# Optimization experiments

Measured on AMD Instinct MI355X. Metric: run time of the kernel, lower is better.

## Reference

```python
import jax, jax.numpy as jnp
import numpy as np

N = 8192          # nodes in batch
D_IN = 512        # in_channels
G = 512           # global_dim
D_OUT = 512       # out_channels
H = 8             # heads
C = 2048          # num_centroids
NUM_NODES = 100000


def setup_inputs() -> dict:
    key = jax.random.key(0)
    ks = jax.random.split(key, 10)
    s = lambda fan_in: 1.0 / np.sqrt(fan_in)
    return {
        "x": jax.random.normal(ks[0], (N, D_IN), jnp.float32),
        "W_proj": jax.random.normal(ks[1], (D_IN, G), jnp.float32) * s(D_IN),
        "b_proj": jnp.zeros((G,), jnp.float32),
        "W_q": jax.random.normal(ks[2], (G, D_OUT), jnp.float32) * s(G),
        "b_q": jnp.zeros((D_OUT,), jnp.float32),
        "W_k": jax.random.normal(ks[3], (G, D_OUT), jnp.float32) * s(G),
        "b_k": jnp.zeros((D_OUT,), jnp.float32),
        "W_v": jax.random.normal(ks[4], (G, D_OUT), jnp.float32) * s(G),
        "b_v": jnp.zeros((D_OUT,), jnp.float32),
        "k_buf": jax.random.normal(ks[5], (C, G), jnp.float32),
        "v_buf": jax.random.normal(ks[6], (C, G), jnp.float32),
        "ln_gamma": jnp.ones((D_OUT,), jnp.float32),
        "ln_beta": jnp.zeros((D_OUT,), jnp.float32),
        "c_idx": jax.random.randint(ks[7], (NUM_NODES,), 0, C, jnp.int64 if jax.config.jax_enable_x64 else jnp.int32),
        "node_indices": jax.random.randint(ks[8], (N,), 0, NUM_NODES, jnp.int64 if jax.config.jax_enable_x64 else jnp.int32),
    }


def _layer_norm(y, gamma, beta, eps=1e-5):
    mu = jnp.mean(y, axis=-1, keepdims=True)
    var = jnp.var(y, axis=-1, keepdims=True)
    return (y - mu) * jax.lax.rsqrt(var + eps) * gamma + beta


def reference(x, W_proj, b_proj, W_q, b_q, W_k, b_k, W_v, b_v,
              k_buf, v_buf, ln_gamma, ln_beta, c_idx, node_indices):
    h, d = H, D_OUT
    dh = d // h
    scale = 1.0 / np.sqrt(d)  # source scales by 1/sqrt(out_channels)

    q_x = x @ W_proj + b_proj                      # [N, G]
    k_x = jax.lax.stop_gradient(k_buf)             # detach().clone()
    v_x = jax.lax.stop_gradient(v_buf)

    # n (h d) -> h n d
    q = (q_x @ W_q + b_q).reshape(-1, h, dh).transpose(1, 0, 2)   # [h, N, dh]
    k = (k_x @ W_k + b_k).reshape(-1, h, dh).transpose(1, 0, 2)   # [h, C, dh]
    v = (v_x @ W_v + b_v).reshape(-1, h, dh).transpose(1, 0, 2)   # [h, C, dh]

    dots = jnp.einsum('hnd,hcd->hnc', q, k) * scale               # [h, N, C]

    # log-count centroid bias (unique/bincount over the full c_idx buffer)
    counts = jnp.bincount(c_idx, length=C)                        # [C] int
    dots = dots + jnp.log(counts.astype(dots.dtype))              # log(0)=-inf masks empty centroids

    attn = jax.nn.softmax(dots, axis=-1)                          # [h, N, C]
    out = jnp.einsum('hnc,hcd->hnd', attn, v)                     # [h, N, dh]
    out = out.transpose(1, 0, 2).reshape(-1, d)                   # [N, d]

    return _layer_norm(out, ln_gamma, ln_beta)
```

## Files before the change

### kernel.cpp

```cpp
#include <hip/hip_runtime.h>
#include <math.h>

typedef __bf16 bf16x8 __attribute__((ext_vector_type(8)));
typedef __bf16 bf16x2 __attribute__((ext_vector_type(2)));
typedef float f32x4 __attribute__((ext_vector_type(4)));
typedef float f32x16 __attribute__((ext_vector_type(16)));
typedef unsigned u32x2v __attribute__((ext_vector_type(2)));
typedef unsigned short u16;

#define NQ 8192
#define DMODEL 512
#define NHEAD 8
#define DH 64
#define NC 2048
#define NIDX 100000

__device__ __forceinline__ u16 f2bf(float f) {
    unsigned u = __float_as_uint(f);
    u += 0x7fffu + ((u >> 16) & 1u);
    return (u16)(u >> 16);
}
__device__ __forceinline__ float bf2f(u16 h) {
    return __uint_as_float(((unsigned)h) << 16);
}
__device__ __forceinline__ unsigned pk2(float a, float b) {
    bf16x2 t; t[0] = (__bf16)a; t[1] = (__bf16)b;
    return __builtin_bit_cast(unsigned, t);
}
__device__ __forceinline__ void plswap(unsigned& a, unsigned& b) {
    u32x2v r = __builtin_amdgcn_permlane32_swap(a, b, false, false);
    a = r[0]; b = r[1];
}
__device__ __forceinline__ int soff(int q, int col) {
    return q * 256 + ((((col >> 2) ^ (q & 7)) << 2) | (col & 3));
}

template <int A_MODE, int B_MODE, int OUT_T>
__device__ __forceinline__ void gemm_bt_body(
    const void* __restrict__ A_, const void* __restrict__ Bt_,
    const float* __restrict__ bias, u16* __restrict__ Cmat,
    int M, int N, int K, int bx, int by)
{
    constexpr int LDP = 40;
    __shared__ __align__(16) u16 As[128 * LDP];
    __shared__ __align__(16) u16 Bs[128 * LDP];
    int tid = threadIdx.x;
    int lane = tid & 63, wid = tid >> 6;
    int wrow = (wid >> 1) * 64, wcol = (wid & 1) * 64;
    int m0 = by * 128, n0 = bx * 128;
    int lr = lane & 15, lg = lane >> 4;
    f32x4 acc[4][4] = {};

    for (int k0 = 0; k0 < K; k0 += 32) {
#pragma unroll
        for (int c = 0; c < 2; c++) {
            int ch = tid + c * 256;
            int row = ch >> 2, colc = (ch & 3) * 8;
            uint4 av;
            if (A_MODE == 1) {
                const float* Af = (const float*)A_;
                float4 a0 = *(const float4*)(Af + (size_t)(m0 + row) * K + k0 + colc);
                float4 a1 = *(const float4*)(Af + (size_t)(m0 + row) * K + k0 + colc + 4);
                av.x = pk2(a0.x, a0.y); av.y = pk2(a0.z, a0.w);
                av.z = pk2(a1.x, a1.y); av.w = pk2(a1.z, a1.w);
            } else if (A_MODE == 2) {
                const float* Af = (const float*)A_;
                float e[8];
#pragma unroll
                for (int i = 0; i < 8; i++)
                    e[i] = Af[(size_t)(k0 + colc + i) * M + m0 + row];
                av.x = pk2(e[0], e[1]); av.y = pk2(e[2], e[3]);
                av.z = pk2(e[4], e[5]); av.w = pk2(e[6], e[7]);
            } else {
                av = *(const uint4*)((const u16*)A_ + (size_t)(m0 + row) * K + k0 + colc);
            }
            *(uint4*)(&As[row * LDP + colc]) = av;
            uint4 bv;
            if (B_MODE == 1) {
                const float* Bf = (const float*)Bt_;
                float4 b0 = *(const float4*)(Bf + (size_t)(n0 + row) * K + k0 + colc);
                float4 b1 = *(const float4*)(Bf + (size_t)(n0 + row) * K + k0 + colc + 4);
                bv.x = pk2(b0.x, b0.y); bv.y = pk2(b0.z, b0.w);
                bv.z = pk2(b1.x, b1.y); bv.w = pk2(b1.z, b1.w);
            } else {
                bv = *(const uint4*)((const u16*)Bt_ + (size_t)(n0 + row) * K + k0 + colc);
            }
            *(uint4*)(&Bs[row * LDP + colc]) = bv;
        }
        __syncthreads();
        bf16x8 af[4], bfr[4];
#pragma unroll
        for (int m = 0; m < 4; m++)
            af[m] = *(const bf16x8*)(&As[(wrow + m * 16 + lr) * LDP + lg * 8]);
#pragma unroll
        for (int n = 0; n < 4; n++)
            bfr[n] = *(const bf16x8*)(&Bs[(wcol + n * 16 + lr) * LDP + lg * 8]);
#pragma unroll
        for (int m = 0; m < 4; m++)
#pragma unroll
            for (int n = 0; n < 4; n++)
                acc[m][n] = __builtin_amdgcn_mfma_f32_16x16x32_bf16(af[m], bfr[n], acc[m][n], 0, 0, 0);
        __syncthreads();
    }
#pragma unroll
    for (int n = 0; n < 4; n++) {
        int col = n0 + wcol + n * 16 + lr;
        float bv = bias ? bias[col] : 0.0f;
#pragma unroll
        for (int m = 0; m < 4; m++) {
            int rbase = m0 + wrow + m * 16 + lg * 4;
            if (OUT_T == 1) {
                int hh = col >> 6, T = (col >> 5) & 1, ql = col & 31;
                int t = rbase >> 5, cc = rbase & 31;
                int u = ((cc >> 4) * 2 + ((cc >> 3) & 1)) * 2 + T;
                size_t off = (size_t)hh * 131072 + (size_t)t * 2048 + u * 256 + ql * 8 + (cc & 7);
                ushort4 o4;
                o4.x = f2bf(acc[m][n][0] + bv);
                o4.y = f2bf(acc[m][n][1] + bv);
                o4.z = f2bf(acc[m][n][2] + bv);
                o4.w = f2bf(acc[m][n][3] + bv);
                *(ushort4*)(Cmat + off) = o4;
            } else if (OUT_T == 2) {
                int hh = col >> 6, m2 = (col >> 4) & 3, h2 = (col >> 3) & 1, jj = col & 7;
                size_t ub = (size_t)hh * 131072 + (size_t)(m2 * 2 + h2) * 256 + jj;
#pragma unroll
                for (int r = 0; r < 4; r++) {
                    int c = rbase + r;
                    Cmat[ub + (size_t)(c >> 5) * 2048 + (c & 31) * 8] = f2bf(acc[m][n][r] + bv);
                }
            } else {
#pragma unroll
                for (int r = 0; r < 4; r++)
                    Cmat[(size_t)(rbase + r) * N + col] = f2bf(acc[m][n][r] + bv);
            }
        }
    }
}

__global__ __launch_bounds__(256) void k_prep2(
    const float* __restrict__ Wq, const float* __restrict__ Wk, const float* __restrict__ Wv,
    const float* __restrict__ Wp, const float* __restrict__ bp, const float* __restrict__ bq_,
    u16* __restrict__ Wk_t, u16* __restrict__ Wv_t,
    u16* __restrict__ WcombT, float* __restrict__ bcomb)
{
    __shared__ float tile[32][33];
    int bid = blockIdx.x, tid = threadIdx.x;
    if (bid < 16) {
        gemm_bt_body<2, 1, 0>(Wq, Wp, nullptr, WcombT, DMODEL, DMODEL, DMODEL,
                              bid & 3, bid >> 2);
    } else if (bid < 18) {
        int j = (bid - 16) * 256 + tid;
        float s = bq_[j];
        for (int k = 0; k < DMODEL; k++) s += bp[k] * Wq[(size_t)k * DMODEL + j];
        bcomb[j] = s;
    } else {
        const float* W; u16* Wt; int tb;
        if (bid < 274) { W = Wk; Wt = Wk_t; tb = bid - 18; }
        else           { W = Wv; Wt = Wv_t; tb = bid - 274; }
        int c0 = (tb & 15) * 32, r0 = (tb >> 4) * 32;
        int tx = tid & 31, ty = tid >> 5;
#pragma unroll
        for (int i = 0; i < 4; i++)
            tile[ty + i * 8][tx] = W[(size_t)(r0 + ty + i * 8) * DMODEL + c0 + tx];
        __syncthreads();
#pragma unroll
        for (int i = 0; i < 4; i++)
            Wt[(size_t)(c0 + ty + i * 8) * DMODEL + r0 + tx] = f2bf(tile[tx][ty + i * 8]);
    }
}

__global__ __launch_bounds__(256) void k_gemm_all(
    const float* __restrict__ kb, const u16* __restrict__ Wkt, const float* __restrict__ bk,
    u16* __restrict__ Kp,
    const float* __restrict__ vb, const u16* __restrict__ Wvt, const float* __restrict__ bv,
    u16* __restrict__ Vp,
    const float* __restrict__ x, const u16* __restrict__ WcombT,
    const float* __restrict__ bcomb, u16* __restrict__ Qm,
    const int* __restrict__ cidx, int* __restrict__ counts)
{
    int b = blockIdx.x;
    if (b < 64)
        gemm_bt_body<1, 0, 2>(kb, Wkt, bk, Kp, NC, DMODEL, DMODEL, b & 3, b >> 2);
    else if (b < 128)
        gemm_bt_body<1, 0, 1>(vb, Wvt, bv, Vp, NC, DMODEL, DMODEL, (b - 64) & 3, (b - 64) >> 2);
    else if (b < 384)
        gemm_bt_body<1, 0, 0>(x, WcombT, bcomb, Qm, NQ, DMODEL, DMODEL, (b - 128) & 3, (b - 128) >> 2);
    else {
        for (int i = (b - 384) * 256 + threadIdx.x; i < NIDX; i += 128 * 256)
            atomicAdd(&counts[cidx[i]], 1);
    }
}

__global__ __launch_bounds__(512, 2) void k_attn8(
    const u16* __restrict__ Q, const u16* __restrict__ Kp, const u16* __restrict__ Vp,
    const int* __restrict__ counts, const float* __restrict__ ln_g,
    const float* __restrict__ ln_b, float* __restrict__ Out, float scale2)
{
    __shared__ float sbias[NC];
    __shared__ unsigned sO[32 * 256];

    int tid = threadIdx.x;
    int lane = tid & 63, wid = tid >> 6;
    int h = wid;
    int ql = lane & 31, hi = lane >> 5;
    int q0 = blockIdx.x * 32;
    int hbase = h * DH;

#pragma unroll
    for (int i = 0; i < 4; i++)
        sbias[tid + i * 512] = log2f((float)counts[tid + i * 512]) - 16.0f;

    bf16x8 qf[4];
#pragma unroll
    for (int m = 0; m < 4; m++)
        qf[m] = *(const bf16x8*)(Q + (size_t)(q0 + ql) * DMODEL + hbase + m * 16 + hi * 8);

    const u16* klane = Kp + (size_t)h * 131072 + hi * 256 + ql * 8;
    const u16* vlane = Vp + (size_t)h * 131072 + hi * 512 + ql * 8;

    bf16x8 kf0[4], kf1[4], vf0[4], vf1[4];
#pragma unroll
    for (int m = 0; m < 4; m++)
        kf0[m] = *(const bf16x8*)(klane + m * 512);
#pragma unroll
    for (int T = 0; T < 2; T++)
#pragma unroll
        for (int ss = 0; ss < 2; ss++)
            vf0[T * 2 + ss] = *(const bf16x8*)(vlane + ss * 1024 + T * 256);

    f32x16 o0 = {}, o1 = {};
    float l_part = 0.f;

    __syncthreads();

    auto body = [&](int t, bf16x8 (&kfc)[4], bf16x8 (&vfc)[4],
                    bf16x8 (&kfn)[4], bf16x8 (&vfn)[4]) {
        f32x4 bq[4];
#pragma unroll
        for (int j = 0; j < 4; j++)
            bq[j] = *(const f32x4*)(sbias + t * 32 + 8 * j + 4 * hi);

        f32x16 acc = {};
        __builtin_amdgcn_s_setprio(1);
#pragma unroll
        for (int m = 0; m < 4; m++)
            acc = __builtin_amdgcn_mfma_f32_32x32x16_bf16(kfc[m], qf[m], acc, 0, 0, 0);
        __builtin_amdgcn_s_setprio(0);

        const u16* kp = klane + (size_t)(t + 1) * 2048;
#pragma unroll
        for (int m = 0; m < 4; m++)
            kfn[m] = *(const bf16x8*)(kp + m * 512);

        unsigned u[8];
        float rs0 = 0.f, rs1 = 0.f;
#pragma unroll
        for (int j = 0; j < 8; j++) {
            float p0 = exp2f(acc[2 * j] * scale2 + bq[(2 * j) >> 2][(2 * j) & 3]);
            float p1 = exp2f(acc[2 * j + 1] * scale2 + bq[(2 * j + 1) >> 2][(2 * j + 1) & 3]);
            rs0 += p0; rs1 += p1;
            u[j] = pk2(p0, p1);
        }
        l_part += rs0 + rs1;

        plswap(u[0], u[2]); plswap(u[1], u[3]);
        plswap(u[4], u[6]); plswap(u[5], u[7]);
        bf16x8 pb0 = __builtin_bit_cast(bf16x8, *(uint4*)&u[0]);
        bf16x8 pb1 = __builtin_bit_cast(bf16x8, *(uint4*)&u[4]);

        __builtin_amdgcn_s_setprio(1);
        o0 = __builtin_amdgcn_mfma_f32_32x32x16_bf16(vfc[0], pb0, o0, 0, 0, 0);
        o0 = __builtin_amdgcn_mfma_f32_32x32x16_bf16(vfc[1], pb1, o0, 0, 0, 0);
        o1 = __builtin_amdgcn_mfma_f32_32x32x16_bf16(vfc[2], pb0, o1, 0, 0, 0);
        o1 = __builtin_amdgcn_mfma_f32_32x32x16_bf16(vfc[3], pb1, o1, 0, 0, 0);
        __builtin_amdgcn_s_setprio(0);

        const u16* vp = vlane + (size_t)(t + 1) * 2048;
#pragma unroll
        for (int T = 0; T < 2; T++)
#pragma unroll
            for (int ss = 0; ss < 2; ss++)
                vfn[T * 2 + ss] = *(const bf16x8*)(vp + ss * 1024 + T * 256);
    };

    for (int t = 0; t < NC / 32; t += 2) {
        body(t,     kf0, vf0, kf1, vf1);
        body(t + 1, kf1, vf1, kf0, vf0);
    }

    float l_tot = l_part + __shfl_xor(l_part, 32);
    float inv = 1.0f / l_tot;

#pragma unroll
    for (int T = 0; T < 2; T++)
#pragma unroll
        for (int j = 0; j < 8; j++) {
            int dw = T * 16 + (j & 1) + 4 * (j >> 1) + 2 * hi;
            float a = (T == 0) ? o0[2 * j] : o1[2 * j];
            float b = (T == 0) ? o0[2 * j + 1] : o1[2 * j + 1];
            sO[soff(ql, h * 32 + dw)] = pk2(a * inv, b * inv);
        }
    __syncthreads();

    float4 g0 = *(const float4*)(ln_g + lane * 8);
    float4 g1 = *(const float4*)(ln_g + lane * 8 + 4);
    float4 b0 = *(const float4*)(ln_b + lane * 8);
    float4 b1 = *(const float4*)(ln_b + lane * 8 + 4);
#pragma unroll
    for (int rr = 0; rr < 4; rr++) {
        int r = wid * 4 + rr;
        uint4 pw = *(const uint4*)(&sO[r * 256 + ((lane ^ (r & 7)) << 2)]);
        float v[8];
        v[0] = bf2f((u16)(pw.x & 0xffff)); v[1] = bf2f((u16)(pw.x >> 16));
        v[2] = bf2f((u16)(pw.y & 0xffff)); v[3] = bf2f((u16)(pw.y >> 16));
        v[4] = bf2f((u16)(pw.z & 0xffff)); v[5] = bf2f((u16)(pw.z >> 16));
        v[6] = bf2f((u16)(pw.w & 0xffff)); v[7] = bf2f((u16)(pw.w >> 16));
        float sum = 0.f, sq = 0.f;
#pragma unroll
        for (int j = 0; j < 8; j++) { sum += v[j]; sq += v[j] * v[j]; }
#pragma unroll
        for (int msk = 1; msk <= 32; msk <<= 1) { sum += __shfl_xor(sum, msk); sq += __shfl_xor(sq, msk); }
        float mu = sum * (1.f / DMODEL);
        float var = sq * (1.f / DMODEL) - mu * mu;
        float rstd = rsqrtf(var + 1e-5f);
        float o[8];
        o[0] = (v[0] - mu) * rstd * g0.x + b0.x; o[1] = (v[1] - mu) * rstd * g0.y + b0.y;
        o[2] = (v[2] - mu) * rstd * g0.z + b0.z; o[3] = (v[3] - mu) * rstd * g0.w + b0.w;
        o[4] = (v[4] - mu) * rstd * g1.x + b1.x; o[5] = (v[5] - mu) * rstd * g1.y + b1.y;
        o[6] = (v[6] - mu) * rstd * g1.z + b1.z; o[7] = (v[7] - mu) * rstd * g1.w + b1.w;
        float* op = Out + (size_t)(q0 + r) * DMODEL + lane * 8;
        *(float4*)op = *(float4*)&o[0];
        *(float4*)(op + 4) = *(float4*)&o[4];
    }
}

extern "C" void kernel_launch(void* const* d_in, const int* in_sizes, int n_in,
                              void* d_out, int out_size, void* d_ws, size_t ws_size,
                              hipStream_t stream)
{
    const float* x      = (const float*)d_in[0];
    const float* W_proj = (const float*)d_in[1];
    const float* b_proj = (const float*)d_in[2];
    const float* W_q    = (const float*)d_in[3];
    const float* b_q    = (const float*)d_in[4];
    const float* W_k    = (const float*)d_in[5];
    const float* b_k    = (const float*)d_in[6];
    const float* W_v    = (const float*)d_in[7];
    const float* b_v    = (const float*)d_in[8];
    const float* k_buf  = (const float*)d_in[9];
    const float* v_buf  = (const float*)d_in[10];
    const float* ln_g   = (const float*)d_in[11];
    const float* ln_b   = (const float*)d_in[12];
    const int*   c_idx  = (const int*)d_in[13];
    float* out = (float*)d_out;

    char* ws = (char*)d_ws;
    size_t off = 0;
    auto alloc = [&](size_t bytes) -> void* {
        void* p = ws + off;
        off += (bytes + 255) & ~(size_t)255;
        return p;
    };
    u16* Wk_t   = (u16*)alloc((size_t)DMODEL * DMODEL * 2);
    u16* Wv_t   = (u16*)alloc((size_t)DMODEL * DMODEL * 2);
    u16* WcombT = (u16*)alloc((size_t)DMODEL * DMODEL * 2);
    u16* Qm     = (u16*)alloc((size_t)NQ * DMODEL * 2);
    u16* Kpm    = (u16*)alloc((size_t)NC * DMODEL * 2);
    u16* Vpm    = (u16*)alloc((size_t)DMODEL * NC * 2);
    int*   counts = (int*)alloc(NC * 4);
    float* bcomb  = (float*)alloc(DMODEL * 4);
    (void)alloc(2200000);

    hipMemsetAsync(counts, 0, NC * 4, stream);

    k_prep2<<<dim3(530), dim3(256), 0, stream>>>(
        W_q, W_k, W_v, W_proj, b_proj, b_q,
        Wk_t, Wv_t, WcombT, bcomb);

    k_gemm_all<<<dim3(512), dim3(256), 0, stream>>>(
        k_buf, Wk_t, b_k, Kpm,
        v_buf, Wv_t, b_v, Vpm,
        x, WcombT, bcomb, Qm,
        c_idx, counts);

    k_attn8<<<dim3(NQ / 32), dim3(512), 0, stream>>>(Qm, Kpm, Vpm, counts, ln_g, ln_b, out, 0.06375872f);
    (void)in_sizes; (void)n_in; (void)out_size; (void)ws_size;
}
```

Baseline: 124.9 us.

## Split centroid dimension across two wave groups per head in attention kernel

Doubles the attention block to 1024 threads so each head gets two waves, each covering half of the 2048 centroids. The partial outputs and row sums are merged through shared memory before normalization and layer norm. This raises the wave count and parallelism per query tile, at the cost of extra shared-memory traffic, more barriers and a bf16-rounded partial sum.

```diff
diff --git a/kernel.cpp b/kernel.cpp
--- a/kernel.cpp
+++ b/kernel.cpp
@@ -191,32 +191,33 @@
     }
 }
 
-__global__ __launch_bounds__(512, 2) void k_attn8(
+__global__ __launch_bounds__(1024, 4) void k_attn9(
     const u16* __restrict__ Q, const u16* __restrict__ Kp, const u16* __restrict__ Vp,
     const int* __restrict__ counts, const float* __restrict__ ln_g,
     const float* __restrict__ ln_b, float* __restrict__ Out, float scale2)
 {
     __shared__ float sbias[NC];
     __shared__ unsigned sO[32 * 256];
+    __shared__ float sl[256];
 
     int tid = threadIdx.x;
     int lane = tid & 63, wid = tid >> 6;
-    int h = wid;
+    int h = wid & 7, hf = wid >> 3;
     int ql = lane & 31, hi = lane >> 5;
     int q0 = blockIdx.x * 32;
     int hbase = h * DH;
 
-#pragma unroll
-    for (int i = 0; i < 4; i++)
-        sbias[tid + i * 512] = log2f((float)counts[tid + i * 512]) - 16.0f;
+    sbias[tid] = log2f((float)counts[tid]) - 16.0f;
+    sbias[tid + 1024] = log2f((float)counts[tid + 1024]) - 16.0f;
 
     bf16x8 qf[4];
 #pragma unroll
     for (int m = 0; m < 4; m++)
         qf[m] = *(const bf16x8*)(Q + (size_t)(q0 + ql) * DMODEL + hbase + m * 16 + hi * 8);
 
-    const u16* klane = Kp + (size_t)h * 131072 + hi * 256 + ql * 8;
-    const u16* vlane = Vp + (size_t)h * 131072 + hi * 512 + ql * 8;
+    const u16* klane = Kp + (size_t)h * 131072 + (size_t)hf * 65536 + hi * 256 + ql * 8;
+    const u16* vlane = Vp + (size_t)h * 131072 + (size_t)hf * 65536 + hi * 512 + ql * 8;
+    int bbase = hf * 1024;
 
     bf16x8 kf0[4], kf1[4], vf0[4], vf1[4];
 #pragma unroll
@@ -238,7 +239,7 @@
         f32x4 bq[4];
 #pragma unroll
         for (int j = 0; j < 4; j++)
-            bq[j] = *(const f32x4*)(sbias + t * 32 + 8 * j + 4 * hi);
+            bq[j] = *(const f32x4*)(sbias + bbase + t * 32 + 8 * j + 4 * hi);
 
         f32x16 acc = {};
         __builtin_amdgcn_s_setprio(1);
@@ -283,23 +284,53 @@
                 vfn[T * 2 + ss] = *(const bf16x8*)(vp + ss * 1024 + T * 256);
     };
 
-    for (int t = 0; t < NC / 32; t += 2) {
+    for (int t = 0; t < NC / 64; t += 2) {
         body(t,     kf0, vf0, kf1, vf1);
         body(t + 1, kf1, vf1, kf0, vf0);
     }
 
     float l_tot = l_part + __shfl_xor(l_part, 32);
-    float inv = 1.0f / l_tot;
-
-#pragma unroll
-    for (int T = 0; T < 2; T++)
-#pragma unroll
-        for (int j = 0; j < 8; j++) {
-            int dw = T * 16 + (j & 1) + 4 * (j >> 1) + 2 * hi;
-            float a = (T == 0) ? o0[2 * j] : o1[2 * j];
-            float b = (T == 0) ? o0[2 * j + 1] : o1[2 * j + 1];
-            sO[soff(ql, h * 32 + dw)] = pk2(a * inv, b * inv);
-        }
+
+    if (hf == 1) {
+#pragma unroll
+        for (int T = 0; T < 2; T++)
+#pragma unroll
+            for (int j = 0; j < 8; j++) {
+                int dw = T * 16 + (j & 1) + 4 * (j >> 1) + 2 * hi;
+                float a = (T == 0) ? o0[2 * j] : o1[2 * j];
+                float b = (T == 0) ? o0[2 * j + 1] : o1[2 * j + 1];
+                sO[(h * 32 + ql) * 32 + dw] = pk2(a, b);
+            }
+        if (hi == 0) sl[h * 32 + ql] = l_tot;
+    }
+    __syncthreads();
+
+    float mrg[32];
+    if (hf == 0) {
+        float inv = 1.0f / (l_tot + sl[h * 32 + ql]);
+#pragma unroll
+        for (int T = 0; T < 2; T++)
+#pragma unroll
+            for (int j = 0; j < 8; j++) {
+                int dw = T * 16 + (j & 1) + 4 * (j >> 1) + 2 * hi;
+                unsigned pv = sO[(h * 32 + ql) * 32 + dw];
+                float a = (T == 0) ? o0[2 * j] : o1[2 * j];
+                float b = (T == 0) ? o0[2 * j + 1] : o1[2 * j + 1];
+                mrg[T * 16 + 2 * j]     = (a + bf2f((u16)(pv & 0xffff))) * inv;
+                mrg[T * 16 + 2 * j + 1] = (b + bf2f((u16)(pv >> 16))) * inv;
+            }
+    }
+    __syncthreads();
+
+    if (hf == 0) {
+#pragma unroll
+        for (int T = 0; T < 2; T++)
+#pragma unroll
+            for (int j = 0; j < 8; j++) {
+                int dw = T * 16 + (j & 1) + 4 * (j >> 1) + 2 * hi;
+                sO[soff(ql, h * 32 + dw)] = pk2(mrg[T * 16 + 2 * j], mrg[T * 16 + 2 * j + 1]);
+            }
+    }
     __syncthreads();
 
     float4 g0 = *(const float4*)(ln_g + lane * 8);
@@ -307,8 +338,8 @@
     float4 b0 = *(const float4*)(ln_b + lane * 8);
     float4 b1 = *(const float4*)(ln_b + lane * 8 + 4);
 #pragma unroll
-    for (int rr = 0; rr < 4; rr++) {
-        int r = wid * 4 + rr;
+    for (int rr = 0; rr < 2; rr++) {
+        int r = wid * 2 + rr;
         uint4 pw = *(const uint4*)(&sO[r * 256 + ((lane ^ (r & 7)) << 2)]);
         float v[8];
         v[0] = bf2f((u16)(pw.x & 0xffff)); v[1] = bf2f((u16)(pw.x >> 16));
@@ -383,6 +414,6 @@
         x, WcombT, bcomb, Qm,
         c_idx, counts);
 
-    k_attn8<<<dim3(NQ / 32), dim3(512), 0, stream>>>(Qm, Kpm, Vpm, counts, ln_g, ln_b, out, 0.06375872f);
+    k_attn9<<<dim3(NQ / 32), dim3(1024), 0, stream>>>(Qm, Kpm, Vpm, counts, ln_g, ln_b, out, 0.06375872f);
     (void)in_sizes; (void)n_in; (void)out_size; (void)ws_size;
 }
```

After: 146.6 us. +17.3%, slower.

## Split attention over centroid halves and merge with separate layernorm kernel

Applied to the files above, without the earlier changes.

Splits the centroid dimension of the attention kernel into two halves via a second grid dimension, doubling the block count. Each half writes unnormalized-by-global partial outputs in bf16 plus row sums, and a new kernel merges the two halves weighted by their sums before applying layernorm. Launch bounds raise the target occupancy to 4 blocks per CU. The aim is better CU utilization with 256 blocks on a many-CU GPU, at the cost of extra global traffic, an extra launch and a second bf16 rounding of the partials. The merge relies on the fixed max bias (no running max), so combining by sums is valid.

```diff
diff --git a/kernel.cpp b/kernel.cpp
--- a/kernel.cpp
+++ b/kernel.cpp
@@ -191,12 +191,12 @@
     }
 }
 
-__global__ __launch_bounds__(512, 2) void k_attn8(
+__global__ __launch_bounds__(512, 4) void k_attn10(
     const u16* __restrict__ Q, const u16* __restrict__ Kp, const u16* __restrict__ Vp,
-    const int* __restrict__ counts, const float* __restrict__ ln_g,
-    const float* __restrict__ ln_b, float* __restrict__ Out, float scale2)
-{
-    __shared__ float sbias[NC];
+    const int* __restrict__ counts, u16* __restrict__ Pp, float* __restrict__ lbuf,
+    float scale2)
+{
+    __shared__ float sbias[NC / 2];
     __shared__ unsigned sO[32 * 256];
 
     int tid = threadIdx.x;
@@ -204,19 +204,19 @@
     int h = wid;
     int ql = lane & 31, hi = lane >> 5;
     int q0 = blockIdx.x * 32;
+    int half = blockIdx.y;
     int hbase = h * DH;
 
-#pragma unroll
-    for (int i = 0; i < 4; i++)
-        sbias[tid + i * 512] = log2f((float)counts[tid + i * 512]) - 16.0f;
+    sbias[tid] = log2f((float)counts[half * 1024 + tid]) - 16.0f;
+    sbias[tid + 512] = log2f((float)counts[half * 1024 + tid + 512]) - 16.0f;
 
     bf16x8 qf[4];
 #pragma unroll
     for (int m = 0; m < 4; m++)
         qf[m] = *(const bf16x8*)(Q + (size_t)(q0 + ql) * DMODEL + hbase + m * 16 + hi * 8);
 
-    const u16* klane = Kp + (size_t)h * 131072 + hi * 256 + ql * 8;
-    const u16* vlane = Vp + (size_t)h * 131072 + hi * 512 + ql * 8;
+    const u16* klane = Kp + (size_t)h * 131072 + (size_t)half * 65536 + hi * 256 + ql * 8;
+    const u16* vlane = Vp + (size_t)h * 131072 + (size_t)half * 65536 + hi * 512 + ql * 8;
 
     bf16x8 kf0[4], kf1[4], vf0[4], vf1[4];
 #pragma unroll
@@ -283,13 +283,16 @@
                 vfn[T * 2 + ss] = *(const bf16x8*)(vp + ss * 1024 + T * 256);
     };
 
-    for (int t = 0; t < NC / 32; t += 2) {
+    for (int t = 0; t < NC / 64; t += 2) {
         body(t,     kf0, vf0, kf1, vf1);
         body(t + 1, kf1, vf1, kf0, vf0);
     }
 
     float l_tot = l_part + __shfl_xor(l_part, 32);
     float inv = 1.0f / l_tot;
+
+    if (hi == 0)
+        lbuf[((size_t)half * NQ + q0 + ql) * NHEAD + h] = l_tot;
 
 #pragma unroll
     for (int T = 0; T < 2; T++)
@@ -302,36 +305,61 @@
         }
     __syncthreads();
 
+#pragma unroll
+    for (int rr = 0; rr < 4; rr++) {
+        int r = wid * 4 + rr;
+        uint4 pw = *(const uint4*)(&sO[r * 256 + ((lane ^ (r & 7)) << 2)]);
+        *(uint4*)(Pp + ((size_t)half * NQ + q0 + r) * DMODEL + lane * 8) = pw;
+    }
+}
+
+__global__ __launch_bounds__(256) void k_mln2(
+    const u16* __restrict__ Pp, const float* __restrict__ lbuf,
+    const float* __restrict__ ln_g, const float* __restrict__ ln_b,
+    float* __restrict__ Out)
+{
+    int lane = threadIdx.x & 63, wid = threadIdx.x >> 6;
+    int q = blockIdx.x * 4 + wid;
+    int hd = lane >> 3;
+
+    float la = lbuf[(size_t)q * NHEAD + hd];
+    float lb = lbuf[((size_t)NQ + q) * NHEAD + hd];
+    float winv = 1.0f / (la + lb);
+    float wa = la * winv, wb = lb * winv;
+
+    uint4 pa = *(const uint4*)(Pp + (size_t)q * DMODEL + lane * 8);
+    uint4 pb = *(const uint4*)(Pp + ((size_t)NQ + q) * DMODEL + lane * 8);
+    float v[8];
+    v[0] = bf2f((u16)(pa.x & 0xffff)) * wa + bf2f((u16)(pb.x & 0xffff)) * wb;
+    v[1] = bf2f((u16)(pa.x >> 16))    * wa + bf2f((u16)(pb.x >> 16))    * wb;
+    v[2] = bf2f((u16)(pa.y & 0xffff)) * wa + bf2f((u16)(pb.y & 0xffff)) * wb;
+    v[3] = bf2f((u16)(pa.y >> 16))    * wa + bf2f((u16)(pb.y >> 16))    * wb;
+    v[4] = bf2f((u16)(pa.z & 0xffff)) * wa + bf2f((u16)(pb.z & 0xffff)) * wb;
+    v[5] = bf2f((u16)(pa.z >> 16))    * wa + bf2f((u16)(pb.z >> 16))    * wb;
+    v[6] = bf2f((u16)(pa.w & 0xffff)) * wa + bf2f((u16)(pb.w & 0xffff)) * wb;
+    v[7] = bf2f((u16)(pa.w >> 16))    * wa + bf2f((u16)(pb.w >> 16))    * wb;
+
+    float sum = 0.f, sq = 0.f;
+#pragma unroll
+    for (int j = 0; j < 8; j++) { sum += v[j]; sq += v[j] * v[j]; }
+#pragma unroll
+    for (int msk = 1; msk <= 32; msk <<= 1) { sum += __shfl_xor(sum, msk); sq += __shfl_xor(sq, msk); }
+    float mu = sum * (1.f / DMODEL);
+    float var = sq * (1.f / DMODEL) - mu * mu;
+    float rstd = rsqrtf(var + 1e-5f);
+
     float4 g0 = *(const float4*)(ln_g + lane * 8);
     float4 g1 = *(const float4*)(ln_g + lane * 8 + 4);
     float4 b0 = *(const float4*)(ln_b + lane * 8);
     float4 b1 = *(const float4*)(ln_b + lane * 8 + 4);
-#pragma unroll
-    for (int rr = 0; rr < 4; rr++) {
-        int r = wid * 4 + rr;
-        uint4 pw = *(const uint4*)(&sO[r * 256 + ((lane ^ (r & 7)) << 2)]);
-        float v[8];
-        v[0] = bf2f((u16)(pw.x & 0xffff)); v[1] = bf2f((u16)(pw.x >> 16));
-        v[2] = bf2f((u16)(pw.y & 0xffff)); v[3] = bf2f((u16)(pw.y >> 16));
-        v[4] = bf2f((u16)(pw.z & 0xffff)); v[5] = bf2f((u16)(pw.z >> 16));
-        v[6] = bf2f((u16)(pw.w & 0xffff)); v[7] = bf2f((u16)(pw.w >> 16));
-        float sum = 0.f, sq = 0.f;
-#pragma unroll
-        for (int j = 0; j < 8; j++) { sum += v[j]; sq += v[j] * v[j]; }
-#pragma unroll
-        for (int msk = 1; msk <= 32; msk <<= 1) { sum += __shfl_xor(sum, msk); sq += __shfl_xor(sq, msk); }
-        float mu = sum * (1.f / DMODEL);
-        float var = sq * (1.f / DMODEL) - mu * mu;
-        float rstd = rsqrtf(var + 1e-5f);
-        float o[8];
-        o[0] = (v[0] - mu) * rstd * g0.x + b0.x; o[1] = (v[1] - mu) * rstd * g0.y + b0.y;
-        o[2] = (v[2] - mu) * rstd * g0.z + b0.z; o[3] = (v[3] - mu) * rstd * g0.w + b0.w;
-        o[4] = (v[4] - mu) * rstd * g1.x + b1.x; o[5] = (v[5] - mu) * rstd * g1.y + b1.y;
-        o[6] = (v[6] - mu) * rstd * g1.z + b1.z; o[7] = (v[7] - mu) * rstd * g1.w + b1.w;
-        float* op = Out + (size_t)(q0 + r) * DMODEL + lane * 8;
-        *(float4*)op = *(float4*)&o[0];
-        *(float4*)(op + 4) = *(float4*)&o[4];
-    }
+    float o[8];
+    o[0] = (v[0] - mu) * rstd * g0.x + b0.x; o[1] = (v[1] - mu) * rstd * g0.y + b0.y;
+    o[2] = (v[2] - mu) * rstd * g0.z + b0.z; o[3] = (v[3] - mu) * rstd * g0.w + b0.w;
+    o[4] = (v[4] - mu) * rstd * g1.x + b1.x; o[5] = (v[5] - mu) * rstd * g1.y + b1.y;
+    o[6] = (v[6] - mu) * rstd * g1.z + b1.z; o[7] = (v[7] - mu) * rstd * g1.w + b1.w;
+    float* op = Out + (size_t)q * DMODEL + lane * 8;
+    *(float4*)op = *(float4*)&o[0];
+    *(float4*)(op + 4) = *(float4*)&o[4];
 }
 
 extern "C" void kernel_launch(void* const* d_in, const int* in_sizes, int n_in,
@@ -369,6 +397,8 @@
     u16* Vpm    = (u16*)alloc((size_t)DMODEL * NC * 2);
     int*   counts = (int*)alloc(NC * 4);
     float* bcomb  = (float*)alloc(DMODEL * 4);
+    u16*   Pp     = (u16*)alloc((size_t)2 * NQ * DMODEL * 2);
+    float* lbuf   = (float*)alloc((size_t)2 * NQ * NHEAD * 4);
     (void)alloc(2200000);
 
     hipMemsetAsync(counts, 0, NC * 4, stream);
@@ -383,6 +413,7 @@
         x, WcombT, bcomb, Qm,
         c_idx, counts);
 
-    k_attn8<<<dim3(NQ / 32), dim3(512), 0, stream>>>(Qm, Kpm, Vpm, counts, ln_g, ln_b, out, 0.06375872f);
+    k_attn10<<<dim3(NQ / 32, 2), dim3(512), 0, stream>>>(Qm, Kpm, Vpm, counts, Pp, lbuf, 0.06375872f);
+    k_mln2<<<dim3(NQ / 4), dim3(256), 0, stream>>>(Pp, lbuf, ln_g, ln_b, out);
     (void)in_sizes; (void)n_in; (void)out_size; (void)ws_size;
 }
```

Result: slower. 133.1 us (+6.5%).
